# Kernel optimization log

Measured on AMD Instinct MI355X. Metric: run time of the kernel, lower is better.

Reference implementation:

```python
import jax, jax.numpy as jnp
import numpy as np

MARGIN = 1.0
EPS = 1e-6  # torch F.pairwise_distance default eps, added elementwise to (x - y)
NEG_INF = -1e30
POS_INF = 1e30


def _pairwise_dist_matrix(e):
    # D[i,j] = || e_i - e_j + EPS ||_2, expanded so we never materialize [B,B,D]:
    # ||d + eps||^2 = ||d||^2 + 2*eps*sum(d) + Dfeat*eps^2,  d = e_i - e_j
    sq = jnp.sum(e * e, axis=1)          # [B]
    s = jnp.sum(e, axis=1)               # [B]
    d2 = (sq[:, None] + sq[None, :] - 2.0 * (e @ e.T)
          + 2.0 * EPS * (s[:, None] - s[None, :])
          + e.shape[1] * (EPS * EPS))
    return jnp.sqrt(jnp.maximum(d2, 0.0))  # [B,B]


def _pdist(x, y):
    # F.pairwise_distance(p=2): ||x - y + eps||
    return jnp.sqrt(jnp.sum(jnp.square(x - y + EPS), axis=-1))


def setup_inputs() -> dict:
    B, D = 4096, 128
    key = jax.random.key(0)
    k1, k2, k3, k4 = jax.random.split(key, 4)
    embedding = jax.random.normal(k1, (B, D), dtype=jnp.float32)
    # label space == batch, each label appears exactly once in the batch
    target_idx = jax.random.permutation(k2, B).astype(jnp.int32)
    positive_idxs = jax.random.bernoulli(k3, 0.02, (B, B))  # [B, L] label-space mask
    negative_idxs = jax.random.bernoulli(k4, 0.5, (B, B))
    return {"embedding": embedding, "target_idx": target_idx,
            "positive_idxs": positive_idxs, "negative_idxs": negative_idxs}


def reference(embedding, target_idx, positive_idxs, negative_idxs):
    # Mining happens under no_grad in the original module.
    dm = jax.lax.stop_gradient(_pairwise_dist_matrix(embedding))  # [B,B]
    # batch j is a positive/negative candidate for anchor i iff its label is flagged
    pos_mask = positive_idxs[:, target_idx]  # [B,B] bool
    neg_mask = negative_idxs[:, target_idx]
    pos_idx = jnp.argmax(jnp.where(pos_mask, dm, NEG_INF), axis=1)  # hardest positive
    neg_idx = jnp.argmin(jnp.where(neg_mask, dm, POS_INF), axis=1)  # hardest negative
    valid = jnp.any(pos_mask, axis=1) & jnp.any(neg_mask, axis=1)
    a = embedding
    p = embedding[pos_idx]
    n = embedding[neg_idx]
    ap = _pdist(a, p)
    an = _pdist(a, n)
    pn = _pdist(p, n)
    loss = jax.nn.relu(ap - jnp.minimum(an, pn) + MARGIN)
    w = valid.astype(loss.dtype)
    return jnp.sum(loss * w) / jnp.maximum(jnp.sum(w), 1.0)
```

## Files before the change

kernel.cpp:

```cpp
#include <hip/hip_runtime.h>
#include <stdint.h>

#define BN 4096
#define DD 128
#define EPSF 1e-6f
#define MARGINF 1.0f

typedef unsigned long long ull;
typedef unsigned short ushort;
typedef short short8 __attribute__((ext_vector_type(8)));
typedef float f32x4 __attribute__((ext_vector_type(4)));

__device__ __forceinline__ unsigned int ord_f32(float f) {
    unsigned int u = __float_as_uint(f);
    return (u & 0x80000000u) ? ~u : (u | 0x80000000u);
}
__device__ __forceinline__ ushort bf16_rne(float x) {
    unsigned int u = __float_as_uint(x);
    return (ushort)((u + 0x7FFFu + ((u >> 16) & 1u)) >> 16);
}

__global__ void k_prep(const float* __restrict__ e, const int* __restrict__ tidx,
                       float* __restrict__ sq, float* __restrict__ s,
                       int* __restrict__ inv, ull* __restrict__ pk, ull* __restrict__ nk,
                       unsigned int* __restrict__ ehi, unsigned int* __restrict__ cnt) {
    int w = threadIdx.x >> 6, lane = threadIdx.x & 63;
    int row = blockIdx.x * 4 + w;
    if (blockIdx.x == 0 && threadIdx.x == 0) cnt[0] = 0u;
    float2 v = ((const float2*)(e + (size_t)row * DD))[lane];
    ushort hx = bf16_rne(v.x), hy = bf16_rne(v.y);
    ehi[row * 64 + lane] = (unsigned int)hx | ((unsigned int)hy << 16);
    float ss = v.x + v.y;
    float qq = v.x * v.x + v.y * v.y;
    #pragma unroll
    for (int off = 32; off > 0; off >>= 1) {
        ss += __shfl_down(ss, off);
        qq += __shfl_down(qq, off);
    }
    if (lane == 0) {
        sq[row] = qq; s[row] = ss;
        inv[tidx[row]] = row;
        pk[row] = 0ULL; nk[row] = 0ULL;
    }
}

__global__ __launch_bounds__(256, 4)
void k_select(const ushort* __restrict__ ehi,
              const int* __restrict__ pos, const int* __restrict__ neg,
              const float* __restrict__ sq, const float* __restrict__ s,
              const int* __restrict__ inv,
              ull* __restrict__ pkey, ull* __restrict__ nkey) {
    __shared__ __align__(16) char smem[36864];
    __shared__ float rjl[128];
    __shared__ int jvs[128];

    const int tid = threadIdx.x;
    const int lane = tid & 63;
    const int w = tid >> 6, wr = w >> 1, wc = w & 1;
    const int lrow = lane & 15, quad = lane >> 4;
    const int i0 = blockIdx.x * 128, c0 = blockIdx.y * 128;

    if (tid < 128) {
        int j = inv[c0 + tid];
        jvs[tid] = j;
        rjl[tid] = sq[j] - 2.0f * EPSF * s[j];
    }
    __syncthreads();

    ushort* Bst = (ushort*)smem;
    #pragma unroll
    for (int it = 0; it < 8; it++) {
        int slot = it * 256 + tid;
        int r = slot >> 4, seg16 = slot & 15;
        int kc = seg16 >> 3, seg = seg16 & 7;
        int jr = jvs[r];
        int4 v = ((const int4*)ehi)[(size_t)jr * 16 + seg16];
        *(int4*)(Bst + (kc * 128 + r) * 72 + seg * 8) = v;
    }
    __syncthreads();

    f32x4 acc[4][4];
    #pragma unroll
    for (int rt = 0; rt < 4; rt++)
        #pragma unroll
        for (int ct = 0; ct < 4; ct++)
            acc[rt][ct] = (f32x4){0.f, 0.f, 0.f, 0.f};

    size_t abase[4];
    #pragma unroll
    for (int rt = 0; rt < 4; rt++)
        abase[rt] = (size_t)(i0 + wr * 64 + rt * 16 + lrow) * DD + quad * 8;

    #pragma unroll
    for (int ks = 0; ks < 4; ks++) {
        const int kc = ks >> 1, ksl = ks & 1;
        short8 ah[4];
        #pragma unroll
        for (int rt = 0; rt < 4; rt++)
            ah[rt] = *(const short8*)(ehi + abase[rt] + ks * 32);
        #pragma unroll
        for (int ct = 0; ct < 4; ct++) {
            const int bo = (kc * 128 + wc * 64 + ct * 16 + lrow) * 72 + ksl * 32 + quad * 8;
            short8 bh = *(const short8*)(Bst + bo);
            #pragma unroll
            for (int rt = 0; rt < 4; rt++)
                acc[rt][ct] = __builtin_amdgcn_mfma_f32_16x16x32_bf16(ah[rt], bh, acc[rt][ct], 0, 0, 0);
        }
    }

    __syncthreads();

    ull* scrp = (ull*)smem;
    ull* scrn = (ull*)(smem + 17408);

    unsigned int jninv[4]; float rjc[4];
    #pragma unroll
    for (int ct = 0; ct < 4; ct++) {
        int cc = wc * 64 + ct * 16 + lrow;
        jninv[ct] = 0xFFFFFFFFu - (unsigned int)jvs[cc];
        rjc[ct] = rjl[cc];
    }

    const size_t mrow0 = (size_t)(i0 + wr * 64 + quad * 4) * BN + (size_t)(c0 + wc * 64 + lrow);
    const int rbase = wr * 64 + quad * 4;

    #pragma unroll
    for (int rt = 0; rt < 4; rt++) {
        #pragma unroll
        for (int t = 0; t < 4; t++) {
            const size_t mb = mrow0 + (size_t)(rt * 16 + t) * BN;
            int pd[4], nd[4];
            #pragma unroll
            for (int ct = 0; ct < 4; ct++) {
                pd[ct] = pos[mb + ct * 16];
                nd[ct] = neg[mb + ct * 16];
            }
            ull kp = 0ULL, kn = 0ULL;
            #pragma unroll
            for (int ct = 0; ct < 4; ct++) {
                float m = rjc[ct] - 2.0f * acc[rt][ct][t];
                unsigned int om = ord_f32(m);
                ull keyp = ((ull)om << 32) | (ull)jninv[ct];
                ull keyn = ((ull)(om ^ 0xFFFFFFFFu) << 32) | (ull)jninv[ct];
                if (pd[ct] != 0 && keyp > kp) kp = keyp;
                if (nd[ct] != 0 && keyn > kn) kn = keyn;
            }
            ull op = __shfl_xor(kp, 8); if (op > kp) kp = op;
            ull on = __shfl_xor(kn, 8); if (on > kn) kn = on;
            if (lrow < 8) {
                const int row = rbase + rt * 16 + t;
                scrp[row * 17 + wc * 8 + lrow] = kp;
                scrn[row * 17 + wc * 8 + lrow] = kn;
            }
        }
    }
    __syncthreads();
    if (tid < 128) {
        ull kp = 0ULL, kn = 0ULL;
        #pragma unroll
        for (int k = 0; k < 16; k++) {
            ull v = scrp[tid * 17 + k]; if (v > kp) kp = v;
            v = scrn[tid * 17 + k];     if (v > kn) kn = v;
        }
        if (kp) atomicMax(&pkey[i0 + tid], kp);
        if (kn) atomicMax(&nkey[i0 + tid], kn);
    }
}

__global__ void k_loss(const float* __restrict__ e,
                       const ull* __restrict__ pkey, const ull* __restrict__ nkey,
                       float* __restrict__ partials, unsigned int* __restrict__ cnt,
                       float* __restrict__ out) {
    int w = threadIdx.x >> 6, lane = threadIdx.x & 63;
    int row = blockIdx.x * 4 + w;
    ull pk = pkey[row], nk = nkey[row];
    float loss = 0.0f, wt = 0.0f;
    if (pk != 0ULL && nk != 0ULL) {
        int pi = (int)(0xFFFFFFFFu - (unsigned)(pk & 0xFFFFFFFFu));
        int ni = (int)(0xFFFFFFFFu - (unsigned)(nk & 0xFFFFFFFFu));
        float2 av = ((const float2*)(e + (size_t)row * DD))[lane];
        float2 pv = ((const float2*)(e + (size_t)pi * DD))[lane];
        float2 nv = ((const float2*)(e + (size_t)ni * DD))[lane];
        float dx, dy;
        dx = av.x - pv.x + EPSF; dy = av.y - pv.y + EPSF;
        float ap2 = dx * dx + dy * dy;
        dx = av.x - nv.x + EPSF; dy = av.y - nv.y + EPSF;
        float an2 = dx * dx + dy * dy;
        dx = pv.x - nv.x + EPSF; dy = pv.y - nv.y + EPSF;
        float pn2 = dx * dx + dy * dy;
        #pragma unroll
        for (int off = 32; off > 0; off >>= 1) {
            ap2 += __shfl_down(ap2, off);
            an2 += __shfl_down(an2, off);
            pn2 += __shfl_down(pn2, off);
        }
        if (lane == 0) {
            float ap = sqrtf(ap2), an = sqrtf(an2), pn = sqrtf(pn2);
            loss = fmaxf(ap - fminf(an, pn) + MARGINF, 0.0f);
            wt = 1.0f;
        }
    }
    __shared__ float sl[4], sw[4];
    __shared__ unsigned int rank;
    if (lane == 0) { sl[w] = loss; sw[w] = wt; }
    __syncthreads();
    if (threadIdx.x == 0) {
        float L = sl[0] + sl[1] + sl[2] + sl[3];
        float W = sw[0] + sw[1] + sw[2] + sw[3];
        __hip_atomic_store(&partials[blockIdx.x * 2 + 0], L, __ATOMIC_RELAXED, __HIP_MEMORY_SCOPE_AGENT);
        __hip_atomic_store(&partials[blockIdx.x * 2 + 1], W, __ATOMIC_RELAXED, __HIP_MEMORY_SCOPE_AGENT);
        __threadfence();
        rank = atomicAdd(cnt, 1u);
    }
    __syncthreads();
    if (rank == (unsigned)(gridDim.x - 1)) {
        __threadfence();
        int tid = threadIdx.x;
        float L = 0.0f, W = 0.0f;
        #pragma unroll
        for (int i = 0; i < 4; i++) {
            int idx = tid + i * 256;
            L += __hip_atomic_load(&partials[idx * 2 + 0], __ATOMIC_RELAXED, __HIP_MEMORY_SCOPE_AGENT);
            W += __hip_atomic_load(&partials[idx * 2 + 1], __ATOMIC_RELAXED, __HIP_MEMORY_SCOPE_AGENT);
        }
        #pragma unroll
        for (int off = 32; off > 0; off >>= 1) {
            L += __shfl_down(L, off);
            W += __shfl_down(W, off);
        }
        __shared__ float fl[4], fw[4];
        int w2 = tid >> 6, l2 = tid & 63;
        if (l2 == 0) { fl[w2] = L; fw[w2] = W; }
        __syncthreads();
        if (tid == 0) {
            float Lt = fl[0] + fl[1] + fl[2] + fl[3];
            float Wt = fw[0] + fw[1] + fw[2] + fw[3];
            out[0] = Lt / fmaxf(Wt, 1.0f);
        }
    }
}

extern "C" void kernel_launch(void* const* d_in, const int* in_sizes, int n_in,
                              void* d_out, int out_size, void* d_ws, size_t ws_size,
                              hipStream_t stream) {
    const float* e    = (const float*)d_in[0];
    const int*   tidx = (const int*)d_in[1];
    const int*   pos  = (const int*)d_in[2];
    const int*   neg  = (const int*)d_in[3];
    float* out = (float*)d_out;

    ull* pkey  = (ull*)d_ws;
    ull* nkey  = pkey + BN;
    float* sq  = (float*)(nkey + BN);
    float* s   = sq + BN;
    int* inv   = (int*)(s + BN);
    float* partials = (float*)(inv + BN);
    unsigned int* ehi = (unsigned int*)(partials + 2048);
    unsigned int* cnt = ehi + (size_t)BN * 64;

    k_prep<<<BN / 4, 256, 0, stream>>>(e, tidx, sq, s, inv, pkey, nkey, ehi, cnt);
    dim3 grid(BN / 128, BN / 128);
    k_select<<<grid, 256, 0, stream>>>((const ushort*)ehi, pos, neg,
                                       sq, s, inv, pkey, nkey);
    k_loss<<<BN / 4, 256, 0, stream>>>(e, pkey, nkey, partials, cnt, out);
}
```

Baseline: 194.1 us.

## Retile selection kernel to 16-row strips with double-buffered column tiles

The selection kernel moves from 128x128 tiles with an LDS-staged B matrix to 16-row blocks that sweep 1024 columns. Each wave loads its B fragments, mask values and per-column constants straight from global memory into registers, double-buffered across 16 column tiles, and keeps running max keys in registers. This lets loads overlap MFMA work and cuts shared memory use and atomics per block. The per-column constants are now precomputed in prep, and the last-block reduction with its counter is replaced by a separate final kernel. In exchange there is an extra launch and less reuse of B across rows, so ehi gathers are re-read by many more blocks.

```diff
diff --git a/kernel.cpp b/kernel.cpp
--- a/kernel.cpp
+++ b/kernel.cpp
@@ -21,12 +21,12 @@
 }
 
 __global__ void k_prep(const float* __restrict__ e, const int* __restrict__ tidx,
-                       float* __restrict__ sq, float* __restrict__ s,
-                       int* __restrict__ inv, ull* __restrict__ pk, ull* __restrict__ nk,
-                       unsigned int* __restrict__ ehi, unsigned int* __restrict__ cnt) {
+                       int* __restrict__ inv, float* __restrict__ rjp,
+                       unsigned int* __restrict__ jn,
+                       ull* __restrict__ pk, ull* __restrict__ nk,
+                       unsigned int* __restrict__ ehi) {
     int w = threadIdx.x >> 6, lane = threadIdx.x & 63;
     int row = blockIdx.x * 4 + w;
-    if (blockIdx.x == 0 && threadIdx.x == 0) cnt[0] = 0u;
     float2 v = ((const float2*)(e + (size_t)row * DD))[lane];
     ushort hx = bf16_rne(v.x), hy = bf16_rne(v.y);
     ehi[row * 64 + lane] = (unsigned int)hx | ((unsigned int)hy << 16);
@@ -38,8 +38,10 @@
         qq += __shfl_down(qq, off);
     }
     if (lane == 0) {
-        sq[row] = qq; s[row] = ss;
-        inv[tidx[row]] = row;
+        int c = tidx[row];
+        inv[c] = row;
+        rjp[c] = qq - 2.0f * EPSF * ss;
+        jn[c] = 0xFFFFFFFFu - (unsigned int)row;
         pk[row] = 0ULL; nk[row] = 0ULL;
     }
 }
@@ -47,130 +49,112 @@
 __global__ __launch_bounds__(256, 4)
 void k_select(const ushort* __restrict__ ehi,
               const int* __restrict__ pos, const int* __restrict__ neg,
-              const float* __restrict__ sq, const float* __restrict__ s,
-              const int* __restrict__ inv,
+              const int* __restrict__ inv, const float* __restrict__ rjp,
+              const unsigned int* __restrict__ jn,
               ull* __restrict__ pkey, ull* __restrict__ nkey) {
-    __shared__ __align__(16) char smem[36864];
-    __shared__ float rjl[128];
-    __shared__ int jvs[128];
+    __shared__ int jvsL[1024];
+    __shared__ float rjL[1024];
+    __shared__ unsigned int jnL[1024];
+    __shared__ ull scrp[16 * 4], scrn[16 * 4];
 
     const int tid = threadIdx.x;
-    const int lane = tid & 63;
-    const int w = tid >> 6, wr = w >> 1, wc = w & 1;
+    const int lane = tid & 63, w = tid >> 6;
     const int lrow = lane & 15, quad = lane >> 4;
-    const int i0 = blockIdx.x * 128, c0 = blockIdx.y * 128;
-
-    if (tid < 128) {
-        int j = inv[c0 + tid];
-        jvs[tid] = j;
-        rjl[tid] = sq[j] - 2.0f * EPSF * s[j];
-    }
-    __syncthreads();
-
-    ushort* Bst = (ushort*)smem;
-    #pragma unroll
-    for (int it = 0; it < 8; it++) {
-        int slot = it * 256 + tid;
-        int r = slot >> 4, seg16 = slot & 15;
-        int kc = seg16 >> 3, seg = seg16 & 7;
-        int jr = jvs[r];
-        int4 v = ((const int4*)ehi)[(size_t)jr * 16 + seg16];
-        *(int4*)(Bst + (kc * 128 + r) * 72 + seg * 8) = v;
-    }
-    __syncthreads();
-
-    f32x4 acc[4][4];
-    #pragma unroll
-    for (int rt = 0; rt < 4; rt++)
-        #pragma unroll
-        for (int ct = 0; ct < 4; ct++)
-            acc[rt][ct] = (f32x4){0.f, 0.f, 0.f, 0.f};
-
-    size_t abase[4];
-    #pragma unroll
-    for (int rt = 0; rt < 4; rt++)
-        abase[rt] = (size_t)(i0 + wr * 64 + rt * 16 + lrow) * DD + quad * 8;
-
-    #pragma unroll
-    for (int ks = 0; ks < 4; ks++) {
-        const int kc = ks >> 1, ksl = ks & 1;
-        short8 ah[4];
-        #pragma unroll
-        for (int rt = 0; rt < 4; rt++)
-            ah[rt] = *(const short8*)(ehi + abase[rt] + ks * 32);
-        #pragma unroll
-        for (int ct = 0; ct < 4; ct++) {
-            const int bo = (kc * 128 + wc * 64 + ct * 16 + lrow) * 72 + ksl * 32 + quad * 8;
-            short8 bh = *(const short8*)(Bst + bo);
-            #pragma unroll
-            for (int rt = 0; rt < 4; rt++)
-                acc[rt][ct] = __builtin_amdgcn_mfma_f32_16x16x32_bf16(ah[rt], bh, acc[rt][ct], 0, 0, 0);
-        }
-    }
-
-    __syncthreads();
-
-    ull* scrp = (ull*)smem;
-    ull* scrn = (ull*)(smem + 17408);
-
-    unsigned int jninv[4]; float rjc[4];
-    #pragma unroll
-    for (int ct = 0; ct < 4; ct++) {
-        int cc = wc * 64 + ct * 16 + lrow;
-        jninv[ct] = 0xFFFFFFFFu - (unsigned int)jvs[cc];
-        rjc[ct] = rjl[cc];
-    }
-
-    const size_t mrow0 = (size_t)(i0 + wr * 64 + quad * 4) * BN + (size_t)(c0 + wc * 64 + lrow);
-    const int rbase = wr * 64 + quad * 4;
-
-    #pragma unroll
-    for (int rt = 0; rt < 4; rt++) {
+    const int r0 = blockIdx.x * 16;
+    const int c0 = blockIdx.y * 1024;
+
+    #pragma unroll
+    for (int k = 0; k < 4; k++) {
+        int idx = k * 256 + tid;
+        jvsL[idx] = inv[c0 + idx];
+        rjL[idx]  = rjp[c0 + idx];
+        jnL[idx]  = jn[c0 + idx];
+    }
+
+    short8 a[4];
+    #pragma unroll
+    for (int ks = 0; ks < 4; ks++)
+        a[ks] = *(const short8*)(ehi + (size_t)(r0 + lrow) * DD + ks * 32 + quad * 8);
+
+    __syncthreads();
+
+    ull kp[4] = {0ULL, 0ULL, 0ULL, 0ULL};
+    ull kn[4] = {0ULL, 0ULL, 0ULL, 0ULL};
+
+    int pm[2][4], nm[2][4];
+    short8 bf[2][4];
+    float rjc[2]; unsigned int jni[2];
+
+#define LOADTILE(BUF, JT) do {                                                 \
+        const int lcol = (JT) * 64 + w * 16 + lrow;                            \
+        const int jr = jvsL[lcol];                                             \
+        rjc[BUF] = rjL[lcol];                                                  \
+        jni[BUF] = jnL[lcol];                                                  \
+        const int* pp = pos + (size_t)(r0 + quad * 4) * BN + (size_t)(c0 + lcol); \
+        const int* np = neg + (size_t)(r0 + quad * 4) * BN + (size_t)(c0 + lcol); \
+        _Pragma("unroll")                                                      \
+        for (int t = 0; t < 4; t++) {                                          \
+            pm[BUF][t] = pp[(size_t)t * BN];                                   \
+            nm[BUF][t] = np[(size_t)t * BN];                                   \
+        }                                                                      \
+        const ushort* bp = ehi + (size_t)jr * DD + quad * 8;                   \
+        _Pragma("unroll")                                                      \
+        for (int ks = 0; ks < 4; ks++)                                         \
+            bf[BUF][ks] = *(const short8*)(bp + ks * 32);                      \
+    } while (0)
+
+    LOADTILE(0, 0);
+
+    #pragma unroll
+    for (int jt = 0; jt < 16; jt++) {
+        const int cur = jt & 1, nxt = cur ^ 1;
+        if (jt < 15) {
+            if (nxt == 0) LOADTILE(0, jt + 1); else LOADTILE(1, jt + 1);
+        }
+        f32x4 acc = (f32x4){0.f, 0.f, 0.f, 0.f};
+        #pragma unroll
+        for (int ks = 0; ks < 4; ks++)
+            acc = __builtin_amdgcn_mfma_f32_16x16x32_bf16(a[ks], bf[cur][ks], acc, 0, 0, 0);
         #pragma unroll
         for (int t = 0; t < 4; t++) {
-            const size_t mb = mrow0 + (size_t)(rt * 16 + t) * BN;
-            int pd[4], nd[4];
-            #pragma unroll
-            for (int ct = 0; ct < 4; ct++) {
-                pd[ct] = pos[mb + ct * 16];
-                nd[ct] = neg[mb + ct * 16];
-            }
-            ull kp = 0ULL, kn = 0ULL;
-            #pragma unroll
-            for (int ct = 0; ct < 4; ct++) {
-                float m = rjc[ct] - 2.0f * acc[rt][ct][t];
-                unsigned int om = ord_f32(m);
-                ull keyp = ((ull)om << 32) | (ull)jninv[ct];
-                ull keyn = ((ull)(om ^ 0xFFFFFFFFu) << 32) | (ull)jninv[ct];
-                if (pd[ct] != 0 && keyp > kp) kp = keyp;
-                if (nd[ct] != 0 && keyn > kn) kn = keyn;
-            }
-            ull op = __shfl_xor(kp, 8); if (op > kp) kp = op;
-            ull on = __shfl_xor(kn, 8); if (on > kn) kn = on;
-            if (lrow < 8) {
-                const int row = rbase + rt * 16 + t;
-                scrp[row * 17 + wc * 8 + lrow] = kp;
-                scrn[row * 17 + wc * 8 + lrow] = kn;
-            }
-        }
-    }
-    __syncthreads();
-    if (tid < 128) {
-        ull kp = 0ULL, kn = 0ULL;
-        #pragma unroll
-        for (int k = 0; k < 16; k++) {
-            ull v = scrp[tid * 17 + k]; if (v > kp) kp = v;
-            v = scrn[tid * 17 + k];     if (v > kn) kn = v;
-        }
-        if (kp) atomicMax(&pkey[i0 + tid], kp);
-        if (kn) atomicMax(&nkey[i0 + tid], kn);
+            float m = rjc[cur] - 2.0f * acc[t];
+            unsigned int om = ord_f32(m);
+            ull keyp = ((ull)om << 32) | (ull)jni[cur];
+            ull keyn = ((ull)(om ^ 0xFFFFFFFFu) << 32) | (ull)jni[cur];
+            if (pm[cur][t] != 0 && keyp > kp[t]) kp[t] = keyp;
+            if (nm[cur][t] != 0 && keyn > kn[t]) kn[t] = keyn;
+        }
+    }
+#undef LOADTILE
+
+    #pragma unroll
+    for (int t = 0; t < 4; t++) {
+        #pragma unroll
+        for (int off = 8; off > 0; off >>= 1) {
+            ull o = __shfl_xor(kp[t], off); if (o > kp[t]) kp[t] = o;
+            o = __shfl_xor(kn[t], off);     if (o > kn[t]) kn[t] = o;
+        }
+        if (lrow == 0) {
+            scrp[(quad * 4 + t) * 4 + w] = kp[t];
+            scrn[(quad * 4 + t) * 4 + w] = kn[t];
+        }
+    }
+    __syncthreads();
+    if (tid < 16) {
+        ull xp = 0ULL, xn = 0ULL;
+        #pragma unroll
+        for (int k = 0; k < 4; k++) {
+            ull v = scrp[tid * 4 + k]; if (v > xp) xp = v;
+            v = scrn[tid * 4 + k];     if (v > xn) xn = v;
+        }
+        if (xp) atomicMax(&pkey[r0 + tid], xp);
+        if (xn) atomicMax(&nkey[r0 + tid], xn);
     }
 }
 
 __global__ void k_loss(const float* __restrict__ e,
                        const ull* __restrict__ pkey, const ull* __restrict__ nkey,
-                       float* __restrict__ partials, unsigned int* __restrict__ cnt,
-                       float* __restrict__ out) {
+                       float* __restrict__ partials) {
     int w = threadIdx.x >> 6, lane = threadIdx.x & 63;
     int row = blockIdx.x * 4 + w;
     ull pk = pkey[row], nk = nkey[row];
@@ -201,42 +185,35 @@
         }
     }
     __shared__ float sl[4], sw[4];
-    __shared__ unsigned int rank;
     if (lane == 0) { sl[w] = loss; sw[w] = wt; }
     __syncthreads();
     if (threadIdx.x == 0) {
-        float L = sl[0] + sl[1] + sl[2] + sl[3];
-        float W = sw[0] + sw[1] + sw[2] + sw[3];
-        __hip_atomic_store(&partials[blockIdx.x * 2 + 0], L, __ATOMIC_RELAXED, __HIP_MEMORY_SCOPE_AGENT);
-        __hip_atomic_store(&partials[blockIdx.x * 2 + 1], W, __ATOMIC_RELAXED, __HIP_MEMORY_SCOPE_AGENT);
-        __threadfence();
-        rank = atomicAdd(cnt, 1u);
-    }
-    __syncthreads();
-    if (rank == (unsigned)(gridDim.x - 1)) {
-        __threadfence();
-        int tid = threadIdx.x;
-        float L = 0.0f, W = 0.0f;
-        #pragma unroll
-        for (int i = 0; i < 4; i++) {
-            int idx = tid + i * 256;
-            L += __hip_atomic_load(&partials[idx * 2 + 0], __ATOMIC_RELAXED, __HIP_MEMORY_SCOPE_AGENT);
-            W += __hip_atomic_load(&partials[idx * 2 + 1], __ATOMIC_RELAXED, __HIP_MEMORY_SCOPE_AGENT);
-        }
-        #pragma unroll
-        for (int off = 32; off > 0; off >>= 1) {
-            L += __shfl_down(L, off);
-            W += __shfl_down(W, off);
-        }
-        __shared__ float fl[4], fw[4];
-        int w2 = tid >> 6, l2 = tid & 63;
-        if (l2 == 0) { fl[w2] = L; fw[w2] = W; }
-        __syncthreads();
-        if (tid == 0) {
-            float Lt = fl[0] + fl[1] + fl[2] + fl[3];
-            float Wt = fw[0] + fw[1] + fw[2] + fw[3];
-            out[0] = Lt / fmaxf(Wt, 1.0f);
-        }
+        partials[blockIdx.x * 2 + 0] = sl[0] + sl[1] + sl[2] + sl[3];
+        partials[blockIdx.x * 2 + 1] = sw[0] + sw[1] + sw[2] + sw[3];
+    }
+}
+
+__global__ void k_final(const float* __restrict__ partials, float* __restrict__ out) {
+    int tid = threadIdx.x;
+    float L = 0.0f, W = 0.0f;
+    for (int i = 0; i < 4; i++) {
+        int idx = tid + i * 256;
+        L += partials[idx * 2];
+        W += partials[idx * 2 + 1];
+    }
+    #pragma unroll
+    for (int off = 32; off > 0; off >>= 1) {
+        L += __shfl_down(L, off);
+        W += __shfl_down(W, off);
+    }
+    __shared__ float sl[4], sw[4];
+    int w = tid >> 6, lane = tid & 63;
+    if (lane == 0) { sl[w] = L; sw[w] = W; }
+    __syncthreads();
+    if (tid == 0) {
+        float Lt = sl[0] + sl[1] + sl[2] + sl[3];
+        float Wt = sw[0] + sw[1] + sw[2] + sw[3];
+        out[0] = Lt / fmaxf(Wt, 1.0f);
     }
 }
 
@@ -251,16 +228,16 @@
 
     ull* pkey  = (ull*)d_ws;
     ull* nkey  = pkey + BN;
-    float* sq  = (float*)(nkey + BN);
-    float* s   = sq + BN;
-    int* inv   = (int*)(s + BN);
-    float* partials = (float*)(inv + BN);
+    int* inv   = (int*)(nkey + BN);
+    float* rjp = (float*)(inv + BN);
+    unsigned int* jn = (unsigned int*)(rjp + BN);
+    float* partials  = (float*)(jn + BN);
     unsigned int* ehi = (unsigned int*)(partials + 2048);
-    unsigned int* cnt = ehi + (size_t)BN * 64;
-
-    k_prep<<<BN / 4, 256, 0, stream>>>(e, tidx, sq, s, inv, pkey, nkey, ehi, cnt);
-    dim3 grid(BN / 128, BN / 128);
+
+    k_prep<<<BN / 4, 256, 0, stream>>>(e, tidx, inv, rjp, jn, pkey, nkey, ehi);
+    dim3 grid(BN / 16, 4);
     k_select<<<grid, 256, 0, stream>>>((const ushort*)ehi, pos, neg,
-                                       sq, s, inv, pkey, nkey);
-    k_loss<<<BN / 4, 256, 0, stream>>>(e, pkey, nkey, partials, cnt, out);
-}
+                                       inv, rjp, jn, pkey, nkey);
+    k_loss<<<BN / 4, 256, 0, stream>>>(e, pkey, nkey, partials);
+    k_final<<<1, 256, 0, stream>>>(partials, out);
+}
```

New measurement: 181.6 us. 1.07x faster.
